# Kernel tuning notes

Hardware: AMD Instinct MI355X
Metric: run time of the kernel (lower is better)

The kernel has to match this reference:

```python
import jax, jax.numpy as jnp
from jax import lax
import numpy as np

VOCAB, EMB, HID, TAGS = 50000, 256, 256, 10
B, S = 32, 256
SOS_IDX, EOS_IDX, PAD_IDX = 1, 2, 0
NEG = -10000.0


def setup_inputs() -> dict:
    key = jax.random.key(0)
    ks = jax.random.split(key, 16)
    x = jax.random.randint(ks[0], (B, S), 0, VOCAB)
    x_lengths = jnp.full((B,), S, dtype=jnp.int32)
    y = jax.random.randint(ks[1], (B, S), 0, TAGS)
    emb = jax.random.normal(ks[2], (VOCAB, EMB), jnp.float32) * 0.1
    emb = emb.at[PAD_IDX].set(0.0)  # padding_idx row is zeros
    k = 1.0 / np.sqrt(HID)
    def u(kk, shp):
        return jax.random.uniform(kk, shp, jnp.float32, -k, k)
    Wih_f = u(ks[3], (4 * HID, EMB)); Whh_f = u(ks[4], (4 * HID, HID))
    bih_f = u(ks[5], (4 * HID,));     bhh_f = u(ks[6], (4 * HID,))
    Wih_b = u(ks[7], (4 * HID, EMB)); Whh_b = u(ks[8], (4 * HID, HID))
    bih_b = u(ks[9], (4 * HID,));     bhh_b = u(ks[10], (4 * HID,))
    Wout = u(ks[11], (TAGS, 2 * HID)); bout = u(ks[12], (TAGS,))
    transitions = jax.random.normal(ks[13], (TAGS, TAGS), jnp.float32)
    transitions = transitions.at[SOS_IDX, :].set(NEG)  # nothing transitions INTO SOS
    transitions = transitions.at[:, EOS_IDX].set(NEG)  # nothing transitions OUT of EOS
    return dict(x=x, x_lengths=x_lengths, y=y, emb=emb,
                Wih_f=Wih_f, Whh_f=Whh_f, bih_f=bih_f, bhh_f=bhh_f,
                Wih_b=Wih_b, Whh_b=Whh_b, bih_b=bih_b, bhh_b=bhh_b,
                Wout=Wout, bout=bout, transitions=transitions)


def _lstm_dir(xs, Wih, Whh, bih, bhh, reverse):
    # xs: [S, B, E] -> hs: [S, B, H]; PyTorch gate order i,f,g,o
    Bsz = xs.shape[1]
    H = Whh.shape[1]
    h0 = jnp.zeros((Bsz, H), xs.dtype)
    c0 = jnp.zeros((Bsz, H), xs.dtype)
    b = bih + bhh
    def step(carry, xt):
        h, c = carry
        g = xt @ Wih.T + h @ Whh.T + b  # [B, 4H]
        i, f, gg, o = jnp.split(g, 4, axis=-1)
        c = jax.nn.sigmoid(f) * c + jax.nn.sigmoid(i) * jnp.tanh(gg)
        h = jax.nn.sigmoid(o) * jnp.tanh(c)
        return (h, c), h
    _, hs = lax.scan(step, (h0, c0), xs, reverse=reverse)
    return hs


def _viterbi(feats, transitions):
    # feats: [L, T]; transitions[to, from]
    T = transitions.shape[0]
    init = jnp.full((T,), NEG, feats.dtype).at[SOS_IDX].set(0.0)
    def step(fv, feat):
        scores = fv[None, :] + transitions          # [to, from]
        bptr = jnp.argmax(scores, axis=1)           # [T]
        fv_new = jnp.max(scores, axis=1) + feat     # [T]
        return fv_new, bptr
    fv, bptrs = lax.scan(step, init, feats)
    terminal = fv + transitions[EOS_IDX]
    best_last = jnp.argmax(terminal)
    path_score = terminal[best_last]
    def back(tag, bp):
        return bp[tag], tag  # carry = previous tag, emit current tag
    _, path = lax.scan(back, best_last, bptrs, reverse=True)  # [L], original order
    return path_score, path


def reference(x, x_lengths, y, emb,
              Wih_f, Whh_f, bih_f, bhh_f,
              Wih_b, Whh_b, bih_b, bhh_b,
              Wout, bout, transitions):
    # embedding lookup; pack/pad with full lengths is identity
    e = emb[x]                       # [B, S, E]
    xs = e.transpose(1, 0, 2)        # [S, B, E]
    hf = _lstm_dir(xs, Wih_f, Whh_f, bih_f, bhh_f, reverse=False)
    hb = _lstm_dir(xs, Wih_b, Whh_b, bih_b, bhh_b, reverse=True)
    h = jnp.concatenate([hf, hb], axis=-1).transpose(1, 0, 2)  # [B, S, 2H]
    out = h.reshape(-1, h.shape[-1]) @ Wout.T + bout            # [B*S, TAGS]
    crf_score, crf_path = _viterbi(out, transitions)            # single decode over flattened seq (faithful)
    return out, crf_score, crf_path
```

## Files before the change

kernel.cpp:

```cpp
#include <hip/hip_runtime.h>
#include <cstdint>
#include <cstddef>

#define S_LEN 256
#define BB    32
#define EMBD  256
#define HID   256
#define NTAG  10
#define L_TOT (BB*S_LEN)
#define NEGV  -10000.0f
#define SOS_I 1
#define EOS_I 2

__device__ __forceinline__ float sigf(float x) { return 1.0f / (1.0f + expf(-x)); }

__global__ __launch_bounds__(256) void prep_all(
    const int* __restrict__ x, const float* __restrict__ emb,
    const float* __restrict__ Wih_f, const float* __restrict__ Whh_f,
    const float* __restrict__ Wih_b, const float* __restrict__ Whh_b,
    const float* __restrict__ bih_f, const float* __restrict__ bhh_f,
    const float* __restrict__ bih_b, const float* __restrict__ bhh_b,
    float* __restrict__ E, float* __restrict__ Wt, float* __restrict__ bc) {
    const int blk = blockIdx.x;
    const int tid = threadIdx.x;
    if (blk < 8192) {
        const int t = blk >> 5, b = blk & 31;
        const int xi = x[b * S_LEN + t];
        E[(size_t)blk * EMBD + tid] = emb[(size_t)xi * EMBD + tid];
    } else if (blk < 8192 + 4096) {
        const int idx = blk - 8192;
        const int dk = idx >> 2;
        const int d = dk >> 9, k = dk & 511;
        const int j = (idx & 3) * 256 + tid;
        const float* src = (d == 0) ? ((k < 256) ? Wih_f : Whh_f)
                                    : ((k < 256) ? Wih_b : Whh_b);
        Wt[(size_t)dk * 1024 + j] = src[(size_t)j * 256 + (k & 255)];
    } else {
        #pragma unroll
        for (int r = 0; r < 8; ++r) {
            const int i = tid + r * 256;
            bc[i] = (i < 1024) ? (bih_f[i] + bhh_f[i]) : (bih_b[i - 1024] + bhh_b[i - 1024]);
        }
    }
}

__global__ __launch_bounds__(1024) void lstm_rec(
    const float* __restrict__ E,
    const float* __restrict__ Wt,
    const float* __restrict__ bc,
    float* __restrict__ hh,
    unsigned long long* __restrict__ mb) {
    const int blk = blockIdx.x;
    const int g   = blk & 15;
    const int mg  = blk >> 4;
    const int d   = g >> 3;
    const int bg  = g & 7;
    const int tid = threadIdx.x;
    const int wave = __builtin_amdgcn_readfirstlane(tid >> 6);
    const int lane = tid & 63;
    const bool is_h = wave >= 8;
    const int wh = wave & 7;
    const int kb = wave * 32;
    const int jg = (lane >> 4) * 256 + mg * 16 + (lane & 15);

    float w[32];
    {
        const float* wsrc = Wt + ((size_t)d * 512 + kb) * 1024 + jg;
        #pragma unroll
        for (int i = 0; i < 32; ++i) w[i] = wsrc[(size_t)i * 1024];
    }

    __shared__ __align__(16) float part[2][4][4][16][20];
    __shared__ __align__(16) float st_e[2][4][256];
    __shared__ __align__(16) float hst[8][4][32];
    __shared__ float cst[4][16];
    __shared__ float bias[64];
    if (tid < 64) bias[tid] = bc[d * 1024 + (tid >> 4) * 256 + mg * 16 + (tid & 15)];

    const int b_l = wave & 3;
    const int so  = (wave >> 2) * 64 + lane;
    const size_t erow = (size_t)(bg * 4 + b_l) * 256 + so;

    {
        const int t0 = d ? (S_LEN - 1) : 0;
        const int t1 = d ? (S_LEN - 2) : 1;
        st_e[0][b_l][so] = E[(size_t)t0 * 8192 + erow];
        st_e[1][b_l][so] = E[(size_t)t1 * 8192 + erow];
    }
    __syncthreads();
    {
        float acc[4] = {0.f, 0.f, 0.f, 0.f};
        if (!is_h) {
            #pragma unroll 2
            for (int i = 0; i < 8; ++i) {
                #pragma unroll
                for (int b = 0; b < 4; ++b) {
                    const float4 v = *(const float4*)&st_e[0][b][kb + i * 4];
                    acc[b] = fmaf(v.x, w[i * 4 + 0], acc[b]);
                    acc[b] = fmaf(v.y, w[i * 4 + 1], acc[b]);
                    acc[b] = fmaf(v.z, w[i * 4 + 2], acc[b]);
                    acc[b] = fmaf(v.w, w[i * 4 + 3], acc[b]);
                }
            }
        }
        #pragma unroll
        for (int b = 0; b < 4; ++b) part[0][b][lane >> 4][lane & 15][wave] = acc[b];
    }

    #pragma unroll 1
    for (int s = 0; s < S_LEN; ++s) {
        __syncthreads();
        const int pc = s & 1, pn = pc ^ 1;

        if (tid < 64) {
            const int bl = tid >> 4, m = tid & 15;
            float vg[4];
            #pragma unroll
            for (int gg = 0; gg < 4; ++gg) {
                const float* pb = &part[pc][bl][gg][m][0];
                const float4 p0 = *(const float4*)(pb + 0);
                const float4 p1 = *(const float4*)(pb + 4);
                const float4 p2 = *(const float4*)(pb + 8);
                const float4 p3 = *(const float4*)(pb + 12);
                vg[gg] = bias[gg * 16 + m]
                       + ((((p0.x + p0.y) + (p0.z + p0.w)) + ((p1.x + p1.y) + (p1.z + p1.w)))
                        + (((p2.x + p2.y) + (p2.z + p2.w)) + ((p3.x + p3.y) + (p3.z + p3.w))));
            }
            const float iv = sigf(vg[0]);
            const float fv = sigf(vg[1]);
            const float gv = tanhf(vg[2]);
            const float ov = sigf(vg[3]);
            float c = (s == 0) ? 0.f : cst[bl][m];
            c = fv * c + iv * gv;
            cst[bl][m] = c;
            const float hv = ov * tanhf(c);
            if (s < S_LEN - 1) {
                const unsigned long long pv =
                    ((unsigned long long)(unsigned)(s + 1) << 32) |
                    (unsigned long long)__float_as_uint(hv);
                __hip_atomic_store(
                    &mb[(((size_t)g * 2 + ((s + 1) & 1)) * 4 + bl) * 256 + mg * 16 + m],
                    pv, __ATOMIC_RELAXED, __HIP_MEMORY_SCOPE_AGENT);
            }
            hh[(((size_t)d * S_LEN + s) * 32 + (bg * 4 + bl)) * 256 + mg * 16 + m] = hv;
        }

        if (s < S_LEN - 1) {
            float acc[4] = {0.f, 0.f, 0.f, 0.f};
            if (!is_h) {
                #pragma unroll 2
                for (int i = 0; i < 8; ++i) {
                    #pragma unroll
                    for (int b = 0; b < 4; ++b) {
                        const float4 v = *(const float4*)&st_e[pn][b][kb + i * 4];
                        acc[b] = fmaf(v.x, w[i * 4 + 0], acc[b]);
                        acc[b] = fmaf(v.y, w[i * 4 + 1], acc[b]);
                        acc[b] = fmaf(v.z, w[i * 4 + 2], acc[b]);
                        acc[b] = fmaf(v.w, w[i * 4 + 3], acc[b]);
                    }
                }
                if (s + 2 < S_LEN) {
                    const int t2 = d ? (S_LEN - 3 - s) : (s + 2);
                    st_e[pc][b_l][so] = E[(size_t)t2 * 8192 + erow];
                }
            } else {
                const unsigned tgt = (unsigned)(s + 1);
                const int bl2 = lane >> 4, kk = (lane & 15) * 2;
                const size_t base = (((size_t)g * 2 + ((s + 1) & 1)) * 4 + bl2) * 256
                                    + wh * 32 + kk;
                unsigned long long a, b;
                while (true) {
                    a = __hip_atomic_load(&mb[base],     __ATOMIC_RELAXED, __HIP_MEMORY_SCOPE_AGENT);
                    b = __hip_atomic_load(&mb[base + 1], __ATOMIC_RELAXED, __HIP_MEMORY_SCOPE_AGENT);
                    const bool ok = ((unsigned)(a >> 32) == tgt) && ((unsigned)(b >> 32) == tgt);
                    if (__all((int)ok)) break;
                }
                hst[wh][bl2][kk]     = __uint_as_float((unsigned)a);
                hst[wh][bl2][kk + 1] = __uint_as_float((unsigned)b);
                #pragma unroll 2
                for (int i = 0; i < 8; ++i) {
                    #pragma unroll
                    for (int b4 = 0; b4 < 4; ++b4) {
                        const float4 v = *(const float4*)&hst[wh][b4][i * 4];
                        acc[b4] = fmaf(v.x, w[i * 4 + 0], acc[b4]);
                        acc[b4] = fmaf(v.y, w[i * 4 + 1], acc[b4]);
                        acc[b4] = fmaf(v.z, w[i * 4 + 2], acc[b4]);
                        acc[b4] = fmaf(v.w, w[i * 4 + 3], acc[b4]);
                    }
                }
            }
            #pragma unroll
            for (int b = 0; b < 4; ++b) part[pn][b][lane >> 4][lane & 15][wave] = acc[b];
        }
    }
}

__global__ __launch_bounds__(128) void out_proj(const float* __restrict__ hh,
                                                const float* __restrict__ Wout,
                                                const float* __restrict__ bout,
                                                float* __restrict__ out) {
    const int r = blockIdx.x * blockDim.x + threadIdx.x;
    const int b = r >> 8, t = r & 255;
    const float* hf = hh + (((size_t)0 * S_LEN + t) * 32 + b) * 256;
    const float* hb = hh + (((size_t)1 * S_LEN + (S_LEN - 1 - t)) * 32 + b) * 256;
    float acc[NTAG];
    #pragma unroll
    for (int q = 0; q < NTAG; ++q) acc[q] = bout[q];
    for (int m = 0; m < HID; ++m) {
        const float hv = hf[m];
        #pragma unroll
        for (int q = 0; q < NTAG; ++q) acc[q] = fmaf(hv, Wout[q * 512 + m], acc[q]);
    }
    for (int m = 0; m < HID; ++m) {
        const float hv = hb[m];
        #pragma unroll
        for (int q = 0; q < NTAG; ++q) acc[q] = fmaf(hv, Wout[q * 512 + 256 + m], acc[q]);
    }
    #pragma unroll
    for (int q = 0; q < NTAG; ++q) out[(size_t)r * NTAG + q] = acc[q];
}

__global__ __launch_bounds__(64) void viterbi_fv(const float* __restrict__ feats,
                                                 const float* __restrict__ trans,
                                                 float* __restrict__ fvh,
                                                 float* __restrict__ score_out,
                                                 int* __restrict__ best_out) {
    const int lane = threadIdx.x;
    float trow[NTAG];
    #pragma unroll
    for (int f = 0; f < NTAG; ++f) trow[f] = (lane < NTAG) ? trans[lane * NTAG + f] : -3.0e38f;
    float fv[NTAG];
    #pragma unroll
    for (int f = 0; f < NTAG; ++f) fv[f] = (f == SOS_I) ? 0.f : NEGV;
    float fq[8];
    #pragma unroll
    for (int q = 0; q < 8; ++q) fq[q] = (lane < NTAG) ? feats[q * NTAG + lane] : 0.f;

    for (int r8 = 0; r8 < L_TOT; r8 += 8) {
        #pragma unroll
        for (int q = 0; q < 8; ++q) {
            const int r = r8 + q;
            float sc[NTAG];
            #pragma unroll
            for (int f = 0; f < NTAG; ++f) sc[f] = fv[f] + trow[f];
            const float m1 = fmaxf(fmaxf(sc[0], sc[1]), sc[2]);
            const float m2 = fmaxf(fmaxf(sc[3], sc[4]), sc[5]);
            const float m3 = fmaxf(fmaxf(sc[6], sc[7]), sc[8]);
            const float mv = fmaxf(fmaxf(fmaxf(m1, m2), m3), sc[9]);
            const float fvnew = mv + fq[q];
            if (lane < NTAG) fvh[(size_t)r * NTAG + lane] = fvnew;
            const int rn = r + 8;
            fq[q] = (rn < L_TOT && lane < NTAG) ? feats[(size_t)rn * NTAG + lane] : 0.f;
            #pragma unroll
            for (int f = 0; f < NTAG; ++f)
                fv[f] = __uint_as_float(__builtin_amdgcn_readlane(__float_as_uint(fvnew), f));
        }
    }

    if (lane == 0) {
        float bm = fv[0] + trans[EOS_I * NTAG + 0];
        int ba = 0;
        #pragma unroll
        for (int f = 1; f < NTAG; ++f) {
            const float tv = fv[f] + trans[EOS_I * NTAG + f];
            if (tv > bm) { bm = tv; ba = f; }
        }
        score_out[0] = bm;
        best_out[0] = ba;
    }
}

__global__ __launch_bounds__(256) void viterbi_bp(const float* __restrict__ fvh,
                                                  const float* __restrict__ trans,
                                                  unsigned int* __restrict__ bp4) {
    const int idx = blockIdx.x * blockDim.x + threadIdx.x;
    if (idx >= (L_TOT / 4) * NTAG) return;
    const int quad = idx / NTAG, to = idx - quad * NTAG;
    float trow[NTAG];
    #pragma unroll
    for (int f = 0; f < NTAG; ++f) trow[f] = trans[to * NTAG + f];
    unsigned pk = 0;
    #pragma unroll
    for (int q = 0; q < 4; ++q) {
        const int r = quad * 4 + q;
        float best = 0.f;
        int arg = 0;
        #pragma unroll
        for (int f = 0; f < NTAG; ++f) {
            const float fp = r ? fvh[(size_t)(r - 1) * NTAG + f]
                               : ((f == SOS_I) ? 0.f : NEGV);
            const float s = fp + trow[f];
            if (f == 0) best = s;
            else if (s > best) { best = s; arg = f; }
        }
        pk |= (unsigned)arg << (q * 8);
    }
    bp4[(size_t)quad * NTAG + to] = pk;
}

__device__ __forceinline__ int bp_at(const unsigned int* bp4, int t, int tag) {
    return (int)((bp4[(size_t)(t >> 2) * NTAG + tag] >> ((t & 3) * 8)) & 0xffu);
}

__global__ __launch_bounds__(1024) void backtrace(const unsigned int* __restrict__ bp4,
                                                  const int* __restrict__ best_in,
                                                  float* __restrict__ path_out) {
    __shared__ unsigned char fc[128 * NTAG];
    __shared__ unsigned char topt[128];
    const int tid = threadIdx.x;
    for (int pe = tid; pe < 128 * NTAG; pe += 1024) {
        const int c = pe / NTAG, e = pe - c * NTAG;
        int cur = e;
        for (int i = 63; i >= 0; --i) cur = bp_at(bp4, c * 64 + i, cur);
        fc[c * NTAG + e] = (unsigned char)cur;
    }
    __syncthreads();
    if (tid == 0) {
        int carry = best_in[0];
        for (int c = 127; c >= 0; --c) {
            topt[c] = (unsigned char)carry;
            carry = fc[c * NTAG + carry];
        }
    }
    __syncthreads();
    for (int c = tid; c < 128; c += 1024) {
        int cur = topt[c];
        for (int i = 63; i >= 0; --i) {
            const int t = c * 64 + i;
            path_out[t] = (float)cur;
            cur = bp_at(bp4, t, cur);
        }
    }
}

extern "C" void kernel_launch(void* const* d_in, const int* in_sizes, int n_in,
                              void* d_out, int out_size, void* d_ws, size_t ws_size,
                              hipStream_t stream) {
    const int*   x     = (const int*)d_in[0];
    const float* emb   = (const float*)d_in[3];
    const float* Wih_f = (const float*)d_in[4];
    const float* Whh_f = (const float*)d_in[5];
    const float* bih_f = (const float*)d_in[6];
    const float* bhh_f = (const float*)d_in[7];
    const float* Wih_b = (const float*)d_in[8];
    const float* Whh_b = (const float*)d_in[9];
    const float* bih_b = (const float*)d_in[10];
    const float* bhh_b = (const float*)d_in[11];
    const float* Wout  = (const float*)d_in[12];
    const float* bout  = (const float*)d_in[13];
    const float* trans = (const float*)d_in[14];

    char* ws = (char*)d_ws;
    size_t off = 0;
    auto alloc = [&](size_t bytes) { void* p = ws + off; off += (bytes + 255) & ~(size_t)255; return p; };
    const size_t MB_BYTES = (size_t)16 * 2 * 4 * 256 * 8;
    unsigned long long* mb = (unsigned long long*)alloc(MB_BYTES);
    int*           best  = (int*)alloc(256);
    float*         E     = (float*)alloc((size_t)L_TOT * EMBD * 4);
    float*         Wt    = (float*)alloc((size_t)2 * 512 * 1024 * 4);
    float*         bc    = (float*)alloc(2048 * 4);
    float*         hh    = (float*)alloc((size_t)2 * S_LEN * BB * HID * 4);
    float*         fvh   = (float*)alloc((size_t)L_TOT * NTAG * 4);
    unsigned*      bp4   = (unsigned*)alloc((size_t)(L_TOT / 4) * NTAG * 4);

    float* out   = (float*)d_out;
    float* score = out + (size_t)L_TOT * NTAG;
    float* path  = score + 1;

    (void)hipMemsetAsync(mb, 0, MB_BYTES, stream);
    hipLaunchKernelGGL(prep_all,  dim3(12289), dim3(256), 0, stream,
                       x, emb, Wih_f, Whh_f, Wih_b, Whh_b,
                       bih_f, bhh_f, bih_b, bhh_b, E, Wt, bc);
    hipLaunchKernelGGL(lstm_rec,  dim3(256),   dim3(1024), 0, stream, E, Wt, bc, hh, mb);
    hipLaunchKernelGGL(out_proj,  dim3(L_TOT / 128), dim3(128), 0, stream, hh, Wout, bout, out);
    hipLaunchKernelGGL(viterbi_fv, dim3(1),    dim3(64),   0, stream, out, trans, fvh, score, best);
    hipLaunchKernelGGL(viterbi_bp, dim3(((L_TOT / 4) * NTAG + 255) / 256), dim3(256), 0, stream,
                       fvh, trans, bp4);
    hipLaunchKernelGGL(backtrace, dim3(1),     dim3(1024), 0, stream, bp4, best, path);
}
```

Before: 1.518 ms.

## Split LSTM recurrence across twice the blocks with two batch rows each

The persistent LSTM recurrence kernel now launches 512 blocks, each handling 2 batch rows instead of 4. This halves per-step FMA work and the amount of h-state each block polls per step, with a swizzled partial-sum layout to cut LDS bank conflicts. The cost is more blocks spinning on the global mailbox, and correctness depends on all 512 1024-thread blocks being co-resident, which the launch bounds hint tries to guarantee. The Viterbi forward kernel also writes 64-wide rows unconditionally so all lanes store without branching, at the cost of a larger scratch buffer.

```diff
diff --git a/kernel.cpp b/kernel.cpp
--- a/kernel.cpp
+++ b/kernel.cpp
@@ -44,17 +44,17 @@
     }
 }
 
-__global__ __launch_bounds__(1024) void lstm_rec(
+__global__ __launch_bounds__(1024, 8) void lstm_rec(
     const float* __restrict__ E,
     const float* __restrict__ Wt,
     const float* __restrict__ bc,
     float* __restrict__ hh,
     unsigned long long* __restrict__ mb) {
     const int blk = blockIdx.x;
-    const int g   = blk & 15;
-    const int mg  = blk >> 4;
-    const int d   = g >> 3;
-    const int bg  = g & 7;
+    const int g   = blk & 31;
+    const int mg  = blk >> 5;
+    const int d   = g >> 4;
+    const int bg  = g & 15;
     const int tid = threadIdx.x;
     const int wave = __builtin_amdgcn_readfirstlane(tid >> 6);
     const int lane = tid & 63;
@@ -70,18 +70,18 @@
         for (int i = 0; i < 32; ++i) w[i] = wsrc[(size_t)i * 1024];
     }
 
-    __shared__ __align__(16) float part[2][4][4][16][20];
-    __shared__ __align__(16) float st_e[2][4][256];
-    __shared__ __align__(16) float hst[8][4][32];
-    __shared__ float cst[4][16];
+    __shared__ __align__(16) float part[2][2][4][324];
+    __shared__ __align__(16) float st_e[2][2][256];
+    __shared__ __align__(16) float hst[8][2][32];
+    __shared__ float cst[2][16];
     __shared__ float bias[64];
     if (tid < 64) bias[tid] = bc[d * 1024 + (tid >> 4) * 256 + mg * 16 + (tid & 15)];
 
-    const int b_l = wave & 3;
-    const int so  = (wave >> 2) * 64 + lane;
-    const size_t erow = (size_t)(bg * 4 + b_l) * 256 + so;
-
-    {
+    const int b_l = wave & 1;
+    const int so  = ((wave >> 1) & 3) * 64 + lane;
+    const size_t erow = (size_t)(bg * 2 + b_l) * 256 + so;
+
+    if (!is_h) {
         const int t0 = d ? (S_LEN - 1) : 0;
         const int t1 = d ? (S_LEN - 2) : 1;
         st_e[0][b_l][so] = E[(size_t)t0 * 8192 + erow];
@@ -89,22 +89,22 @@
     }
     __syncthreads();
     {
-        float acc[4] = {0.f, 0.f, 0.f, 0.f};
+        float a0 = 0.f, a1 = 0.f;
         if (!is_h) {
             #pragma unroll 2
             for (int i = 0; i < 8; ++i) {
-                #pragma unroll
-                for (int b = 0; b < 4; ++b) {
-                    const float4 v = *(const float4*)&st_e[0][b][kb + i * 4];
-                    acc[b] = fmaf(v.x, w[i * 4 + 0], acc[b]);
-                    acc[b] = fmaf(v.y, w[i * 4 + 1], acc[b]);
-                    acc[b] = fmaf(v.z, w[i * 4 + 2], acc[b]);
-                    acc[b] = fmaf(v.w, w[i * 4 + 3], acc[b]);
-                }
+                const float4 v0 = *(const float4*)&st_e[0][0][kb + i * 4];
+                const float4 v1 = *(const float4*)&st_e[0][1][kb + i * 4];
+                a0 = fmaf(v0.x, w[i*4+0], a0); a0 = fmaf(v0.y, w[i*4+1], a0);
+                a0 = fmaf(v0.z, w[i*4+2], a0); a0 = fmaf(v0.w, w[i*4+3], a0);
+                a1 = fmaf(v1.x, w[i*4+0], a1); a1 = fmaf(v1.y, w[i*4+1], a1);
+                a1 = fmaf(v1.z, w[i*4+2], a1); a1 = fmaf(v1.w, w[i*4+3], a1);
             }
         }
-        #pragma unroll
-        for (int b = 0; b < 4; ++b) part[0][b][lane >> 4][lane & 15][wave] = acc[b];
+        const int gq = lane >> 4, m = lane & 15;
+        const int slot = wave ^ (m & 3);
+        part[0][0][gq][m * 20 + slot] = a0;
+        part[0][1][gq][m * 20 + slot] = a1;
     }
 
     #pragma unroll 1
@@ -112,12 +112,12 @@
         __syncthreads();
         const int pc = s & 1, pn = pc ^ 1;
 
-        if (tid < 64) {
+        if (tid < 32) {
             const int bl = tid >> 4, m = tid & 15;
             float vg[4];
             #pragma unroll
             for (int gg = 0; gg < 4; ++gg) {
-                const float* pb = &part[pc][bl][gg][m][0];
+                const float* pb = &part[pc][bl][gg][m * 20];
                 const float4 p0 = *(const float4*)(pb + 0);
                 const float4 p1 = *(const float4*)(pb + 4);
                 const float4 p2 = *(const float4*)(pb + 8);
@@ -139,25 +139,23 @@
                     ((unsigned long long)(unsigned)(s + 1) << 32) |
                     (unsigned long long)__float_as_uint(hv);
                 __hip_atomic_store(
-                    &mb[(((size_t)g * 2 + ((s + 1) & 1)) * 4 + bl) * 256 + mg * 16 + m],
+                    &mb[(((size_t)g * 2 + ((s + 1) & 1)) * 2 + bl) * 256 + mg * 16 + m],
                     pv, __ATOMIC_RELAXED, __HIP_MEMORY_SCOPE_AGENT);
             }
-            hh[(((size_t)d * S_LEN + s) * 32 + (bg * 4 + bl)) * 256 + mg * 16 + m] = hv;
+            hh[(((size_t)d * S_LEN + s) * 32 + (bg * 2 + bl)) * 256 + mg * 16 + m] = hv;
         }
 
         if (s < S_LEN - 1) {
-            float acc[4] = {0.f, 0.f, 0.f, 0.f};
+            float a0 = 0.f, a1 = 0.f;
             if (!is_h) {
                 #pragma unroll 2
                 for (int i = 0; i < 8; ++i) {
-                    #pragma unroll
-                    for (int b = 0; b < 4; ++b) {
-                        const float4 v = *(const float4*)&st_e[pn][b][kb + i * 4];
-                        acc[b] = fmaf(v.x, w[i * 4 + 0], acc[b]);
-                        acc[b] = fmaf(v.y, w[i * 4 + 1], acc[b]);
-                        acc[b] = fmaf(v.z, w[i * 4 + 2], acc[b]);
-                        acc[b] = fmaf(v.w, w[i * 4 + 3], acc[b]);
-                    }
+                    const float4 v0 = *(const float4*)&st_e[pn][0][kb + i * 4];
+                    const float4 v1 = *(const float4*)&st_e[pn][1][kb + i * 4];
+                    a0 = fmaf(v0.x, w[i*4+0], a0); a0 = fmaf(v0.y, w[i*4+1], a0);
+                    a0 = fmaf(v0.z, w[i*4+2], a0); a0 = fmaf(v0.w, w[i*4+3], a0);
+                    a1 = fmaf(v1.x, w[i*4+0], a1); a1 = fmaf(v1.y, w[i*4+1], a1);
+                    a1 = fmaf(v1.z, w[i*4+2], a1); a1 = fmaf(v1.w, w[i*4+3], a1);
                 }
                 if (s + 2 < S_LEN) {
                     const int t2 = d ? (S_LEN - 3 - s) : (s + 2);
@@ -165,32 +163,29 @@
                 }
             } else {
                 const unsigned tgt = (unsigned)(s + 1);
-                const int bl2 = lane >> 4, kk = (lane & 15) * 2;
-                const size_t base = (((size_t)g * 2 + ((s + 1) & 1)) * 4 + bl2) * 256
+                const int bl2 = lane >> 5, kk = lane & 31;
+                const size_t base = (((size_t)g * 2 + ((s + 1) & 1)) * 2 + bl2) * 256
                                     + wh * 32 + kk;
-                unsigned long long a, b;
+                unsigned long long v;
                 while (true) {
-                    a = __hip_atomic_load(&mb[base],     __ATOMIC_RELAXED, __HIP_MEMORY_SCOPE_AGENT);
-                    b = __hip_atomic_load(&mb[base + 1], __ATOMIC_RELAXED, __HIP_MEMORY_SCOPE_AGENT);
-                    const bool ok = ((unsigned)(a >> 32) == tgt) && ((unsigned)(b >> 32) == tgt);
-                    if (__all((int)ok)) break;
+                    v = __hip_atomic_load(&mb[base], __ATOMIC_RELAXED, __HIP_MEMORY_SCOPE_AGENT);
+                    if (__all((int)((unsigned)(v >> 32) == tgt))) break;
                 }
-                hst[wh][bl2][kk]     = __uint_as_float((unsigned)a);
-                hst[wh][bl2][kk + 1] = __uint_as_float((unsigned)b);
+                hst[wh][bl2][kk] = __uint_as_float((unsigned)v);
                 #pragma unroll 2
                 for (int i = 0; i < 8; ++i) {
-                    #pragma unroll
-                    for (int b4 = 0; b4 < 4; ++b4) {
-                        const float4 v = *(const float4*)&hst[wh][b4][i * 4];
-                        acc[b4] = fmaf(v.x, w[i * 4 + 0], acc[b4]);
-                        acc[b4] = fmaf(v.y, w[i * 4 + 1], acc[b4]);
-                        acc[b4] = fmaf(v.z, w[i * 4 + 2], acc[b4]);
-                        acc[b4] = fmaf(v.w, w[i * 4 + 3], acc[b4]);
-                    }
+                    const float4 v0 = *(const float4*)&hst[wh][0][i * 4];
+                    const float4 v1 = *(const float4*)&hst[wh][1][i * 4];
+                    a0 = fmaf(v0.x, w[i*4+0], a0); a0 = fmaf(v0.y, w[i*4+1], a0);
+                    a0 = fmaf(v0.z, w[i*4+2], a0); a0 = fmaf(v0.w, w[i*4+3], a0);
+                    a1 = fmaf(v1.x, w[i*4+0], a1); a1 = fmaf(v1.y, w[i*4+1], a1);
+                    a1 = fmaf(v1.z, w[i*4+2], a1); a1 = fmaf(v1.w, w[i*4+3], a1);
                 }
             }
-            #pragma unroll
-            for (int b = 0; b < 4; ++b) part[pn][b][lane >> 4][lane & 15][wave] = acc[b];
+            const int gq = lane >> 4, m = lane & 15;
+            const int slot = wave ^ (m & 3);
+            part[pn][0][gq][m * 20 + slot] = a0;
+            part[pn][1][gq][m * 20 + slot] = a1;
         }
     }
 }
@@ -222,19 +217,21 @@
 
 __global__ __launch_bounds__(64) void viterbi_fv(const float* __restrict__ feats,
                                                  const float* __restrict__ trans,
-                                                 float* __restrict__ fvh,
+                                                 float* __restrict__ fvh64,
                                                  float* __restrict__ score_out,
                                                  int* __restrict__ best_out) {
     const int lane = threadIdx.x;
+    const int flane = (lane < NTAG) ? lane : (NTAG - 1);
     float trow[NTAG];
     #pragma unroll
-    for (int f = 0; f < NTAG; ++f) trow[f] = (lane < NTAG) ? trans[lane * NTAG + f] : -3.0e38f;
+    for (int f = 0; f < NTAG; ++f)
+        trow[f] = (lane < NTAG) ? trans[lane * NTAG + f] : -3.0e38f;
     float fv[NTAG];
     #pragma unroll
     for (int f = 0; f < NTAG; ++f) fv[f] = (f == SOS_I) ? 0.f : NEGV;
     float fq[8];
     #pragma unroll
-    for (int q = 0; q < 8; ++q) fq[q] = (lane < NTAG) ? feats[q * NTAG + lane] : 0.f;
+    for (int q = 0; q < 8; ++q) fq[q] = feats[q * NTAG + flane];
 
     for (int r8 = 0; r8 < L_TOT; r8 += 8) {
         #pragma unroll
@@ -248,9 +245,9 @@
             const float m3 = fmaxf(fmaxf(sc[6], sc[7]), sc[8]);
             const float mv = fmaxf(fmaxf(fmaxf(m1, m2), m3), sc[9]);
             const float fvnew = mv + fq[q];
-            if (lane < NTAG) fvh[(size_t)r * NTAG + lane] = fvnew;
+            fvh64[(size_t)r * 64 + lane] = fvnew;
             const int rn = r + 8;
-            fq[q] = (rn < L_TOT && lane < NTAG) ? feats[(size_t)rn * NTAG + lane] : 0.f;
+            if (rn < L_TOT) fq[q] = feats[(size_t)rn * NTAG + flane];
             #pragma unroll
             for (int f = 0; f < NTAG; ++f)
                 fv[f] = __uint_as_float(__builtin_amdgcn_readlane(__float_as_uint(fvnew), f));
@@ -270,7 +267,7 @@
     }
 }
 
-__global__ __launch_bounds__(256) void viterbi_bp(const float* __restrict__ fvh,
+__global__ __launch_bounds__(256) void viterbi_bp(const float* __restrict__ fvh64,
                                                   const float* __restrict__ trans,
                                                   unsigned int* __restrict__ bp4) {
     const int idx = blockIdx.x * blockDim.x + threadIdx.x;
@@ -287,7 +284,7 @@
         int arg = 0;
         #pragma unroll
         for (int f = 0; f < NTAG; ++f) {
-            const float fp = r ? fvh[(size_t)(r - 1) * NTAG + f]
+            const float fp = r ? fvh64[(size_t)(r - 1) * 64 + f]
                                : ((f == SOS_I) ? 0.f : NEGV);
             const float s = fp + trow[f];
             if (f == 0) best = s;
@@ -353,14 +350,14 @@
     char* ws = (char*)d_ws;
     size_t off = 0;
     auto alloc = [&](size_t bytes) { void* p = ws + off; off += (bytes + 255) & ~(size_t)255; return p; };
-    const size_t MB_BYTES = (size_t)16 * 2 * 4 * 256 * 8;
+    const size_t MB_BYTES = (size_t)32 * 2 * 2 * 256 * 8;
     unsigned long long* mb = (unsigned long long*)alloc(MB_BYTES);
     int*           best  = (int*)alloc(256);
     float*         E     = (float*)alloc((size_t)L_TOT * EMBD * 4);
     float*         Wt    = (float*)alloc((size_t)2 * 512 * 1024 * 4);
     float*         bc    = (float*)alloc(2048 * 4);
     float*         hh    = (float*)alloc((size_t)2 * S_LEN * BB * HID * 4);
-    float*         fvh   = (float*)alloc((size_t)L_TOT * NTAG * 4);
+    float*         fvh64 = (float*)alloc((size_t)L_TOT * 64 * 4);
     unsigned*      bp4   = (unsigned*)alloc((size_t)(L_TOT / 4) * NTAG * 4);
 
     float* out   = (float*)d_out;
@@ -371,10 +368,10 @@
     hipLaunchKernelGGL(prep_all,  dim3(12289), dim3(256), 0, stream,
                        x, emb, Wih_f, Whh_f, Wih_b, Whh_b,
                        bih_f, bhh_f, bih_b, bhh_b, E, Wt, bc);
-    hipLaunchKernelGGL(lstm_rec,  dim3(256),   dim3(1024), 0, stream, E, Wt, bc, hh, mb);
+    hipLaunchKernelGGL(lstm_rec,  dim3(512),   dim3(1024), 0, stream, E, Wt, bc, hh, mb);
     hipLaunchKernelGGL(out_proj,  dim3(L_TOT / 128), dim3(128), 0, stream, hh, Wout, bout, out);
-    hipLaunchKernelGGL(viterbi_fv, dim3(1),    dim3(64),   0, stream, out, trans, fvh, score, best);
+    hipLaunchKernelGGL(viterbi_fv, dim3(1),    dim3(64),   0, stream, out, trans, fvh64, score, best);
     hipLaunchKernelGGL(viterbi_bp, dim3(((L_TOT / 4) * NTAG + 255) / 256), dim3(256), 0, stream,
-                       fvh, trans, bp4);
+                       fvh64, trans, bp4);
     hipLaunchKernelGGL(backtrace, dim3(1),     dim3(1024), 0, stream, bp4, best, path);
 }
```

New measurement: 3.338 ms. 2.2x slower.
